# Kernel optimization log

Measured on AMD Instinct MI355X. Metric: run time of the kernel, lower is better.

Reference implementation:

```python
import jax, jax.numpy as jnp
import numpy as np

HEADS = 16  # module init arg `heads`


def setup_inputs() -> dict:
    key = jax.random.key(0)
    k1, k2, k3 = jax.random.split(key, 3)
    B, T, D = 2, 2048, 1024
    x = jax.random.normal(k1, (B, T, D), dtype=jnp.float32)
    w_qkv = jax.random.normal(k2, (D, 3 * D), dtype=jnp.float32) * (1.0 / np.sqrt(D))
    w_proj = jax.random.normal(k3, (D, D), dtype=jnp.float32) * (1.0 / np.sqrt(D))
    b_proj = jnp.zeros((D,), dtype=jnp.float32)
    return {"x": x, "w_qkv": w_qkv, "w_proj": w_proj, "b_proj": b_proj,
            "window": 16, "stride": 16}


def reference(x, w_qkv, w_proj, b_proj, window, stride):
    B, T, D = x.shape
    H = HEADS
    hd = D // H
    scale = 1.0 / np.sqrt(hd)

    qkv = x @ w_qkv                              # [B,T,3D]
    qkv = qkv.reshape(B, T, 3, H, hd)
    q = jnp.transpose(qkv[:, :, 0], (0, 2, 1, 3))  # [B,H,T,hd]
    k = jnp.transpose(qkv[:, :, 1], (0, 2, 1, 3))
    v = jnp.transpose(qkv[:, :, 2], (0, 2, 1, 3))

    # Local window attention: pad front with zeros (matches F.pad), gather
    # sliding windows so patches[..., t, w, :] = k_padded[..., t + w, :].
    pad = window - 1
    k_pad = jnp.pad(k, ((0, 0), (0, 0), (pad, 0), (0, 0)))
    v_pad = jnp.pad(v, ((0, 0), (0, 0), (pad, 0), (0, 0)))
    win_idx = jnp.arange(T)[:, None] + jnp.arange(window)[None, :]  # [T,W]
    pk = k_pad[:, :, win_idx]                    # [B,H,T,W,hd]
    pv = v_pad[:, :, win_idx]                    # [B,H,T,W,hd]

    attn_local = jnp.einsum('bhtd,bhtwd->bhtw', q, pk) * scale
    attn_local = jax.nn.softmax(attn_local, axis=-1)  # zero-pad keys included, as in torch
    out_local = jnp.einsum('bhtw,bhtwd->bhtd', attn_local, pv)

    # Strided global attention
    g_idx = jnp.arange(0, T, stride)
    kg = k[:, :, g_idx]                          # [B,H,G,hd]
    vg = v[:, :, g_idx]
    attn_g = jnp.einsum('bhtd,bhgd->bhtg', q, kg) * scale
    attn_g = jax.nn.softmax(attn_g, axis=-1)
    out_global = jnp.einsum('bhtg,bhgd->bhtd', attn_g, vg)

    out = out_local + out_global                 # [B,H,T,hd]
    out = jnp.transpose(out, (0, 2, 1, 3)).reshape(B, T, D)
    return out @ w_proj + b_proj
```

## Files before the change

kernel.cpp:

```cpp
#include <hip/hip_runtime.h>
#include <hip/hip_bf16.h>

#define BB 2
#define TT 2048
#define DD 1024
#define HH 16
#define HD 64
#define WIN 16
#define NG 128
#define QKVLD 3072

typedef __bf16 bf16x8 __attribute__((ext_vector_type(8)));
typedef _Float16 f16x8 __attribute__((ext_vector_type(8)));
typedef float f32x4 __attribute__((ext_vector_type(4)));
typedef _Float16 h2 __attribute__((ext_vector_type(2)));
typedef __fp16 pk2_t __attribute__((ext_vector_type(2)));

__device__ __forceinline__ unsigned short f2bf(float f) {
    union { float f; unsigned int i; } x; x.f = f;
    unsigned int r = x.i + 0x7FFFu + ((x.i >> 16) & 1u);
    return (unsigned short)(r >> 16);
}
__device__ __forceinline__ unsigned short f2h(float f) {
    union { _Float16 h; unsigned short u; } x; x.h = (_Float16)f; return x.u;
}
__device__ __forceinline__ unsigned int pk2h(float lo, float hi) {
    union { pk2_t h; unsigned int u; } X;
    X.h = __builtin_amdgcn_cvt_pkrtz(lo, hi);
    return X.u;
}

__device__ __forceinline__ void gll16(const unsigned short* g, unsigned short* l) {
    __builtin_amdgcn_global_load_lds(
        (const __attribute__((address_space(1))) void*)g,
        (__attribute__((address_space(3))) void*)l,
        16, 0, 0);
}

__global__ __launch_bounds__(256) void prepass_kernel(
    const float* __restrict__ x,
    const float* __restrict__ w_qkv,
    const float* __restrict__ w_proj,
    unsigned short* __restrict__ xb,
    unsigned short* __restrict__ wqkvT,
    unsigned short* __restrict__ wprojT)
{
    __shared__ float tile[64][65];
    const int bid = blockIdx.x;
    const int tid = threadIdx.x;

    if (bid < 2048) {
        const size_t i = ((size_t)bid * 256 + tid) * 8;
        float4 f0 = *(const float4*)(x + i);
        float4 f1 = *(const float4*)(x + i + 4);
        ushort4 a = { f2bf(f0.x), f2bf(f0.y), f2bf(f0.z), f2bf(f0.w) };
        ushort4 b = { f2bf(f1.x), f2bf(f1.y), f2bf(f1.z), f2bf(f1.w) };
        *(ushort4*)(xb + i) = a;
        *(ushort4*)(xb + i + 4) = b;
        return;
    }

    const float* w;
    unsigned short* wT;
    int nblk, kblk, N;
    if (bid < 2816) {
        const int b2 = bid - 2048;
        w = w_qkv; wT = wqkvT; N = 3072;
        nblk = b2 % 48; kblk = b2 / 48;
    } else {
        const int b2 = bid - 2816;
        w = w_proj; wT = wprojT; N = 1024;
        nblk = b2 % 16; kblk = b2 / 16;
    }
    const int K = 1024;
    const int n0 = nblk * 64, k0 = kblk * 64;

    {
        const int krow = tid >> 2;
        const int nc0  = (tid & 3) * 16;
        const float* src = w + (size_t)(k0 + krow) * N + n0 + nc0;
        float4 f0 = *(const float4*)(src);
        float4 f1 = *(const float4*)(src + 4);
        float4 f2 = *(const float4*)(src + 8);
        float4 f3 = *(const float4*)(src + 12);
        *(float4*)&tile[krow][nc0]      = f0;
        *(float4*)&tile[krow][nc0 + 4]  = f1;
        *(float4*)&tile[krow][nc0 + 8]  = f2;
        *(float4*)&tile[krow][nc0 + 12] = f3;
    }
    __syncthreads();
    #pragma unroll
    for (int rep = 0; rep < 2; ++rep) {
        const int n   = (tid >> 3) + rep * 32;
        const int kc0 = (tid & 7) * 8;
        union { uint4 v; unsigned short u[8]; } o;
        #pragma unroll
        for (int j = 0; j < 8; ++j) o.u[j] = f2bf(tile[kc0 + j][n]);
        *(uint4*)(wT + (size_t)(n0 + n) * K + k0 + kc0) = o.v;
    }
}

template<int MODE, int TN>
__global__ __launch_bounds__(256) void gemm_kernel(
    const unsigned short* __restrict__ A,
    const unsigned short* __restrict__ Bt,
    void* __restrict__ Cp,
    const float* __restrict__ bias,
    int M, int N, int K)
{
    constexpr int NJ = TN / 32;
    constexpr int BRW = TN / 4;
    __shared__ __align__(16) unsigned short As[128 * 64];
    __shared__ __align__(16) unsigned short Bs[TN * 64];
    const int tid  = threadIdx.x;
    const int wave = tid >> 6;
    const int lane = tid & 63;
    const int lm   = lane & 15;
    const int quad = lane >> 4;
    const int wm   = (wave >> 1) * 64;
    const int wn   = (wave & 1) * (TN / 2);
    const int bm   = blockIdx.y * 128;
    const int bn   = blockIdx.x * TN;

    f32x4 acc[4][NJ];
    const f32x4 z4 = { 0.f, 0.f, 0.f, 0.f };
    #pragma unroll
    for (int i = 0; i < 4; ++i)
        #pragma unroll
        for (int j = 0; j < NJ; ++j) acc[i][j] = z4;

    const int lrow = lane >> 3;
    const int lcol = ((lane & 7) ^ lrow) * 8;
    const unsigned short* gA = A  + (size_t)(bm + wave * 32  + lrow) * K + lcol;
    const unsigned short* gB = Bt + (size_t)(bn + wave * BRW + lrow) * K + lcol;
    unsigned short* lA = &As[(wave * 32)  * 64];
    unsigned short* lB = &Bs[(wave * BRW) * 64];

    const int sx = lm & 7;
    for (int k0 = 0; k0 < K; k0 += 64) {
        __syncthreads();
        #pragma unroll
        for (int s = 0; s < 4; ++s)
            gll16(gA + k0 + (size_t)(8 * s) * K, lA + (8 * s) * 64);
        #pragma unroll
        for (int s = 0; s < BRW / 8; ++s)
            gll16(gB + k0 + (size_t)(8 * s) * K, lB + (8 * s) * 64);
        __syncthreads();
        #pragma unroll
        for (int kk = 0; kk < 2; ++kk) {
            bf16x8 af[4], bfr[NJ];
            #pragma unroll
            for (int i = 0; i < 4; ++i)
                af[i] = *(const bf16x8*)&As[(wm + i * 16 + lm) * 64
                                            + (((kk * 4 + quad) ^ sx) * 8)];
            #pragma unroll
            for (int j = 0; j < NJ; ++j)
                bfr[j] = *(const bf16x8*)&Bs[(wn + j * 16 + lm) * 64
                                             + (((kk * 4 + quad) ^ sx) * 8)];
            #pragma unroll
            for (int i = 0; i < 4; ++i)
                #pragma unroll
                for (int j = 0; j < NJ; ++j)
                    acc[i][j] = __builtin_amdgcn_mfma_f32_16x16x32_bf16(
                        af[i], bfr[j], acc[i][j], 0, 0, 0);
        }
    }

    #pragma unroll
    for (int i = 0; i < 4; ++i) {
        #pragma unroll
        for (int r = 0; r < 4; ++r) {
            const int row = bm + wm + i * 16 + quad * 4 + r;
            #pragma unroll
            for (int j = 0; j < NJ; ++j) {
                const int col = bn + wn + j * 16 + lm;
                float v = acc[i][j][r];
                if constexpr (MODE == 0) {
                    ((unsigned short*)Cp)[(size_t)row * N + col] = f2h(v);
                } else {
                    ((float*)Cp)[(size_t)row * N + col] = v + bias[col];
                }
            }
        }
    }
}

__device__ __forceinline__ f16x8 pfrag(unsigned int fa0, unsigned int fa1,
                                       unsigned int fb0, unsigned int fb1,
                                       int quad) {
    const unsigned int t16_0 = (quad == 2) ? fb0 : fa0;
    const unsigned int t16_1 = (quad == 2) ? fb1 : fa1;
    const unsigned int t32_0 = (quad == 0) ? fb0 : fa0;
    const unsigned int t32_1 = (quad == 0) ? fb1 : fa1;
    const unsigned int t48_0 = (quad == 1) ? fb0 : fa0;
    const unsigned int t48_1 = (quad == 1) ? fb1 : fa1;
    const unsigned int s16_0 = (unsigned int)__shfl_xor((int)t16_0, 16, 64);
    const unsigned int s16_1 = (unsigned int)__shfl_xor((int)t16_1, 16, 64);
    const unsigned int s32_0 = (unsigned int)__shfl_xor((int)t32_0, 32, 64);
    const unsigned int s32_1 = (unsigned int)__shfl_xor((int)t32_1, 32, 64);
    const unsigned int s48_0 = (unsigned int)__shfl_xor((int)t48_0, 48, 64);
    const unsigned int s48_1 = (unsigned int)__shfl_xor((int)t48_1, 48, 64);
    unsigned int w0, w1, w2, w3;
    if (quad == 0)      { w0 = fa0;   w1 = fa1;   w2 = s16_0; w3 = s16_1; }
    else if (quad == 1) { w0 = s48_0; w1 = s48_1; w2 = s32_0; w3 = s32_1; }
    else if (quad == 2) { w0 = s32_0; w1 = s32_1; w2 = s48_0; w3 = s48_1; }
    else                { w0 = s16_0; w1 = s16_1; w2 = fb0;   w3 = fb1;   }
    union { unsigned int u[4]; f16x8 v; } R;
    R.u[0] = w0; R.u[1] = w1; R.u[2] = w2; R.u[3] = w3;
    return R.v;
}

__global__ __launch_bounds__(256, 4) void attn_kernel(
    const unsigned short* __restrict__ qkv,
    unsigned short* __restrict__ attn_out)
{
    __shared__ __align__(16) unsigned short smem[14976];
    unsigned short* const Kg  = smem;
    unsigned short* const Kl  = smem + 9216;
    unsigned short* const VgT = smem;
    unsigned short* const VlT = smem + 8704;
    unsigned short* const Ep  = smem + 9216;

    const int tid  = threadIdx.x;
    const int wave = tid >> 6;
    const int lane = tid & 63;
    const int lm   = lane & 15;
    const int quad = lane >> 4;
    const int bx   = blockIdx.x;
    const int bh   = bx >> 5;
    const int t0   = (bx & 31) * 64;
    const int b    = bh >> 4;
    const int h    = bh & 15;

    const size_t baseQ = (size_t)(b * TT) * QKVLD + h * HD;

    const int r  = tid >> 1;
    const int hf = tid & 1;
    uint4 vg[4], vl[4];
    {
        const unsigned short* ks = qkv + baseQ + 1024 + (size_t)(16 * r) * QKVLD + hf * 32;
        const unsigned short* vs = ks + 1024;
        unsigned short* kd = Kg + r * 72 + hf * 32;
        #pragma unroll
        for (int j = 0; j < 4; ++j) *(uint4*)(kd + j * 8) = *(const uint4*)(ks + j * 8);
        #pragma unroll
        for (int j = 0; j < 4; ++j) vg[j] = *(const uint4*)(vs + j * 8);

        if (r < 80) {
            const int tl = t0 - 15 + r;
            unsigned short* kld = Kl + r * 72 + hf * 32;
            if (tl < 0 || tl >= TT) {
                const uint4 z = { 0, 0, 0, 0 };
                #pragma unroll
                for (int j = 0; j < 4; ++j) { *(uint4*)(kld + j * 8) = z; vl[j] = z; }
            } else {
                const unsigned short* kls = qkv + baseQ + 1024 + (size_t)tl * QKVLD + hf * 32;
                const unsigned short* vls = kls + 1024;
                #pragma unroll
                for (int j = 0; j < 4; ++j) *(uint4*)(kld + j * 8) = *(const uint4*)(kls + j * 8);
                #pragma unroll
                for (int j = 0; j < 4; ++j) vl[j] = *(const uint4*)(vls + j * 8);
            }
        }
    }

    f16x8 qf[2];
    {
        const unsigned short* qrow = qkv + baseQ + (size_t)(t0 + 16 * wave + lm) * QKVLD;
        const h2 sc = { (_Float16)0.125f, (_Float16)0.125f };
        #pragma unroll
        for (int c = 0; c < 2; ++c) {
            union { uint4 u; h2 hh[4]; f16x8 v; } U;
            U.u = *(const uint4*)(qrow + c * 32 + quad * 8);
            #pragma unroll
            for (int k = 0; k < 4; ++k) U.hh[k] *= sc;
            qf[c] = U.v;
        }
    }

    __syncthreads();

    f32x4 sg[8], sl[2];
    const f32x4 z4 = { 0.f, 0.f, 0.f, 0.f };
    #pragma unroll
    for (int f = 0; f < 8; ++f) sg[f] = z4;
    sl[0] = z4; sl[1] = z4;
    __builtin_amdgcn_s_setprio(1);
    #pragma unroll
    for (int f = 0; f < 8; ++f)
        #pragma unroll
        for (int c = 0; c < 2; ++c)
            sg[f] = __builtin_amdgcn_mfma_f32_16x16x32_f16(
                *(const f16x8*)&Kg[(16 * f + lm) * 72 + c * 32 + quad * 8], qf[c],
                sg[f], 0, 0, 0);
    #pragma unroll
    for (int f = 0; f < 2; ++f)
        #pragma unroll
        for (int c = 0; c < 2; ++c)
            sl[f] = __builtin_amdgcn_mfma_f32_16x16x32_f16(
                *(const f16x8*)&Kl[(16 * wave + 16 * f + lm) * 72 + c * 32 + quad * 8], qf[c],
                sl[f], 0, 0, 0);
    __builtin_amdgcn_s_setprio(0);

    float invg, invl;
    {
        float dg = 0.f, dl = 0.f;
        #pragma unroll
        for (int f = 0; f < 8; ++f)
            #pragma unroll
            for (int rr = 0; rr < 4; ++rr) {
                float e = __expf(sg[f][rr]); sg[f][rr] = e; dg += e;
            }
        #pragma unroll
        for (int f = 0; f < 2; ++f)
            #pragma unroll
            for (int rr = 0; rr < 4; ++rr) {
                const int j2 = 16 * f + quad * 4 + rr;
                const bool in = (j2 >= lm) && (j2 <= lm + 15);
                float e = in ? __expf(sl[f][rr]) : 0.f;
                sl[f][rr] = e; dl += e;
            }
        dg += __shfl_xor(dg, 16, 64);
        dg += __shfl_xor(dg, 32, 64);
        dl += __shfl_xor(dl, 16, 64);
        dl += __shfl_xor(dl, 32, 64);
        invg = 1.f / dg;
        invl = 1.f / dl;
    }

    f16x8 pa0, pa1, pa2, pa3, pal;
    {
        #pragma unroll
        for (int f = 0; f < 8; ++f)
            #pragma unroll
            for (int rr = 0; rr < 4; ++rr) sg[f][rr] *= invg;
        #pragma unroll
        for (int f = 0; f < 2; ++f)
            #pragma unroll
            for (int rr = 0; rr < 4; ++rr) sl[f][rr] *= invl;
        pa0 = pfrag(pk2h(sg[0][0], sg[0][1]), pk2h(sg[0][2], sg[0][3]),
                    pk2h(sg[1][0], sg[1][1]), pk2h(sg[1][2], sg[1][3]), quad);
        pa1 = pfrag(pk2h(sg[2][0], sg[2][1]), pk2h(sg[2][2], sg[2][3]),
                    pk2h(sg[3][0], sg[3][1]), pk2h(sg[3][2], sg[3][3]), quad);
        pa2 = pfrag(pk2h(sg[4][0], sg[4][1]), pk2h(sg[4][2], sg[4][3]),
                    pk2h(sg[5][0], sg[5][1]), pk2h(sg[5][2], sg[5][3]), quad);
        pa3 = pfrag(pk2h(sg[6][0], sg[6][1]), pk2h(sg[6][2], sg[6][3]),
                    pk2h(sg[7][0], sg[7][1]), pk2h(sg[7][2], sg[7][3]), quad);
        pal = pfrag(pk2h(sl[0][0], sl[0][1]), pk2h(sl[0][2], sl[0][3]),
                    pk2h(sl[1][0], sl[1][1]), pk2h(sl[1][2], sl[1][3]), quad);
    }

    __syncthreads();

    {
        union { uint4 u[4]; unsigned short s[32]; } Ug;
        #pragma unroll
        for (int j = 0; j < 4; ++j) Ug.u[j] = vg[j];
        #pragma unroll
        for (int j = 0; j < 32; ++j) VgT[(hf * 32 + j) * 136 + r] = Ug.s[j];
        if (r < 80) {
            union { uint4 u[4]; unsigned short s[32]; } Ul;
            #pragma unroll
            for (int j = 0; j < 4; ++j) Ul.u[j] = vl[j];
            #pragma unroll
            for (int j = 0; j < 32; ++j) VlT[(hf * 32 + j) * 88 + r] = Ul.s[j];
        }
    }

    __syncthreads();

    f32x4 o[4];
    #pragma unroll
    for (int c = 0; c < 4; ++c) o[c] = z4;
    __builtin_amdgcn_s_setprio(1);
    #pragma unroll
    for (int c = 0; c < 4; ++c) {
        o[c] = __builtin_amdgcn_mfma_f32_16x16x32_f16(
            pa0, *(const f16x8*)&VgT[(16 * c + lm) * 136 + 0 * 32 + quad * 8], o[c], 0, 0, 0);
        o[c] = __builtin_amdgcn_mfma_f32_16x16x32_f16(
            pa1, *(const f16x8*)&VgT[(16 * c + lm) * 136 + 1 * 32 + quad * 8], o[c], 0, 0, 0);
        o[c] = __builtin_amdgcn_mfma_f32_16x16x32_f16(
            pa2, *(const f16x8*)&VgT[(16 * c + lm) * 136 + 2 * 32 + quad * 8], o[c], 0, 0, 0);
        o[c] = __builtin_amdgcn_mfma_f32_16x16x32_f16(
            pa3, *(const f16x8*)&VgT[(16 * c + lm) * 136 + 3 * 32 + quad * 8], o[c], 0, 0, 0);
        o[c] = __builtin_amdgcn_mfma_f32_16x16x32_f16(
            pal, *(const f16x8*)&VlT[(16 * c + lm) * 88 + 16 * wave + quad * 8], o[c], 0, 0, 0);
    }
    __builtin_amdgcn_s_setprio(0);

    __syncthreads();

    {
        unsigned short* const Pw = Ep + wave * (16 * 72);
        #pragma unroll
        for (int rr = 0; rr < 4; ++rr) {
            unsigned short* orow_p = Pw + (quad * 4 + rr) * 72;
            #pragma unroll
            for (int c = 0; c < 4; ++c) orow_p[16 * c + lm] = f2bf(o[c][rr]);
        }
        const int orow = lane >> 2;
        const int ocol = (lane & 3) * 16;
        const uint4 d0 = *(const uint4*)&Pw[orow * 72 + ocol];
        const uint4 d1 = *(const uint4*)&Pw[orow * 72 + ocol + 8];
        unsigned short* dst = attn_out + (size_t)(b * TT + t0 + 16 * wave + orow) * DD + h * HD + ocol;
        *(uint4*)(dst)     = d0;
        *(uint4*)(dst + 8) = d1;
    }
}

extern "C" void kernel_launch(void* const* d_in, const int* in_sizes, int n_in,
                              void* d_out, int out_size, void* d_ws, size_t ws_size,
                              hipStream_t stream) {
    const float* x      = (const float*)d_in[0];
    const float* w_qkv  = (const float*)d_in[1];
    const float* w_proj = (const float*)d_in[2];
    const float* b_proj = (const float*)d_in[3];

    char* ws = (char*)d_ws;
    unsigned short* qkv    = (unsigned short*)ws;
    unsigned short* xb     = (unsigned short*)(ws + 25165824);
    unsigned short* attnb  = xb;
    unsigned short* wqkvT  = (unsigned short*)(ws + 25165824 + 8388608);
    unsigned short* wprojT = (unsigned short*)(ws + 25165824 + 8388608 + 6291456);
    float* out = (float*)d_out;

    prepass_kernel<<<3072, 256, 0, stream>>>(x, w_qkv, w_proj, xb, wqkvT, wprojT);

    gemm_kernel<0, 128><<<dim3(3072 / 128, 4096 / 128), 256, 0, stream>>>(
        xb, wqkvT, qkv, nullptr, 4096, 3072, 1024);

    attn_kernel<<<dim3(BB * HH * (TT / 64)), 256, 0, stream>>>(qkv, attnb);

    gemm_kernel<1, 64><<<dim3(1024 / 64, 4096 / 128), 256, 0, stream>>>(
        attnb, wprojT, out, b_proj, 4096, 1024, 1024);
}
```

Baseline: 148.7 us.

## Double attention query block to 128 rows with 512 threads; widen proj GEMM tile

The attention kernel now processes 128 query rows per block with 8 waves instead of 64 rows with 4 waves. The global strided K/V tile is then loaded and transposed once for twice as many queries, which halves redundant global-key traffic. Local K/V staging is split across thread halves, and an extra 16-row tail is loaded by the first 32 threads. The output projection GEMM also moves from a 64 to a 128 N-tile, leaving fewer blocks (256 instead of 512), which may reduce occupancy and load balance.

```diff
diff --git a/kernel.cpp b/kernel.cpp
--- a/kernel.cpp
+++ b/kernel.cpp
@@ -9,6 +9,7 @@
 #define WIN 16
 #define NG 128
 #define QKVLD 3072
+#define QB 128
 
 typedef __bf16 bf16x8 __attribute__((ext_vector_type(8)));
 typedef _Float16 f16x8 __attribute__((ext_vector_type(8)));
@@ -210,16 +211,16 @@
     return R.v;
 }
 
-__global__ __launch_bounds__(256, 4) void attn_kernel(
+__global__ __launch_bounds__(512, 4) void attn_kernel(
     const unsigned short* __restrict__ qkv,
     unsigned short* __restrict__ attn_out)
 {
-    __shared__ __align__(16) unsigned short smem[14976];
+    __shared__ __align__(16) unsigned short smem[19584];
     unsigned short* const Kg  = smem;
     unsigned short* const Kl  = smem + 9216;
     unsigned short* const VgT = smem;
-    unsigned short* const VlT = smem + 8704;
-    unsigned short* const Ep  = smem + 9216;
+    unsigned short* const VlT = smem + 9216;
+    unsigned short* const Ep  = smem;
 
     const int tid  = threadIdx.x;
     const int wave = tid >> 6;
@@ -227,40 +228,52 @@
     const int lm   = lane & 15;
     const int quad = lane >> 4;
     const int bx   = blockIdx.x;
-    const int bh   = bx >> 5;
-    const int t0   = (bx & 31) * 64;
+    const int bh   = bx >> 4;
+    const int t0   = (bx & 15) * QB;
     const int b    = bh >> 4;
     const int h    = bh & 15;
 
     const size_t baseQ = (size_t)(b * TT) * QKVLD + h * HD;
 
-    const int r  = tid >> 1;
+    const int r  = (tid & 255) >> 1;
     const int hf = tid & 1;
-    uint4 vg[4], vl[4];
-    {
+    uint4 va[4];
+    if (tid < 256) {
         const unsigned short* ks = qkv + baseQ + 1024 + (size_t)(16 * r) * QKVLD + hf * 32;
         const unsigned short* vs = ks + 1024;
         unsigned short* kd = Kg + r * 72 + hf * 32;
         #pragma unroll
         for (int j = 0; j < 4; ++j) *(uint4*)(kd + j * 8) = *(const uint4*)(ks + j * 8);
         #pragma unroll
-        for (int j = 0; j < 4; ++j) vg[j] = *(const uint4*)(vs + j * 8);
-
-        if (r < 80) {
-            const int tl = t0 - 15 + r;
-            unsigned short* kld = Kl + r * 72 + hf * 32;
-            if (tl < 0 || tl >= TT) {
-                const uint4 z = { 0, 0, 0, 0 };
-                #pragma unroll
-                for (int j = 0; j < 4; ++j) { *(uint4*)(kld + j * 8) = z; vl[j] = z; }
-            } else {
-                const unsigned short* kls = qkv + baseQ + 1024 + (size_t)tl * QKVLD + hf * 32;
-                const unsigned short* vls = kls + 1024;
-                #pragma unroll
-                for (int j = 0; j < 4; ++j) *(uint4*)(kld + j * 8) = *(const uint4*)(kls + j * 8);
-                #pragma unroll
-                for (int j = 0; j < 4; ++j) vl[j] = *(const uint4*)(vls + j * 8);
-            }
+        for (int j = 0; j < 4; ++j) va[j] = *(const uint4*)(vs + j * 8);
+    } else {
+        const int tl = t0 - 15 + r;
+        unsigned short* kld = Kl + r * 72 + hf * 32;
+        if (tl < 0 || tl >= TT) {
+            const uint4 z = { 0, 0, 0, 0 };
+            #pragma unroll
+            for (int j = 0; j < 4; ++j) { *(uint4*)(kld + j * 8) = z; va[j] = z; }
+        } else {
+            const unsigned short* kls = qkv + baseQ + 1024 + (size_t)tl * QKVLD + hf * 32;
+            const unsigned short* vls = kls + 1024;
+            #pragma unroll
+            for (int j = 0; j < 4; ++j) *(uint4*)(kld + j * 8) = *(const uint4*)(kls + j * 8);
+            #pragma unroll
+            for (int j = 0; j < 4; ++j) va[j] = *(const uint4*)(vls + j * 8);
+        }
+    }
+    if (tid < 32) {
+        const int r2 = 128 + (tid >> 1);
+        const int tl = t0 - 15 + r2;
+        unsigned short* kld = Kl + r2 * 72 + hf * 32;
+        if (tl < 0 || tl >= TT) {
+            const uint4 z = { 0, 0, 0, 0 };
+            #pragma unroll
+            for (int j = 0; j < 4; ++j) *(uint4*)(kld + j * 8) = z;
+        } else {
+            const unsigned short* kls = qkv + baseQ + 1024 + (size_t)tl * QKVLD + hf * 32;
+            #pragma unroll
+            for (int j = 0; j < 4; ++j) *(uint4*)(kld + j * 8) = *(const uint4*)(kls + j * 8);
         }
     }
 
@@ -353,17 +366,31 @@
     __syncthreads();
 
     {
-        union { uint4 u[4]; unsigned short s[32]; } Ug;
-        #pragma unroll
-        for (int j = 0; j < 4; ++j) Ug.u[j] = vg[j];
-        #pragma unroll
-        for (int j = 0; j < 32; ++j) VgT[(hf * 32 + j) * 136 + r] = Ug.s[j];
-        if (r < 80) {
-            union { uint4 u[4]; unsigned short s[32]; } Ul;
-            #pragma unroll
-            for (int j = 0; j < 4; ++j) Ul.u[j] = vl[j];
-            #pragma unroll
-            for (int j = 0; j < 32; ++j) VlT[(hf * 32 + j) * 88 + r] = Ul.s[j];
+        union { uint4 u[4]; unsigned short s[32]; } U;
+        #pragma unroll
+        for (int j = 0; j < 4; ++j) U.u[j] = va[j];
+        if (tid < 256) {
+            #pragma unroll
+            for (int j = 0; j < 32; ++j) VgT[(hf * 32 + j) * 136 + r] = U.s[j];
+        } else {
+            #pragma unroll
+            for (int j = 0; j < 32; ++j) VlT[(hf * 32 + j) * 152 + r] = U.s[j];
+        }
+        if (tid < 32) {
+            const int r2 = 128 + (tid >> 1);
+            const int tl = t0 - 15 + r2;
+            union { uint4 u[4]; unsigned short s[32]; } W;
+            if (tl < 0 || tl >= TT) {
+                const uint4 z = { 0, 0, 0, 0 };
+                #pragma unroll
+                for (int j = 0; j < 4; ++j) W.u[j] = z;
+            } else {
+                const unsigned short* vls = qkv + baseQ + 2048 + (size_t)tl * QKVLD + hf * 32;
+                #pragma unroll
+                for (int j = 0; j < 4; ++j) W.u[j] = *(const uint4*)(vls + j * 8);
+            }
+            #pragma unroll
+            for (int j = 0; j < 32; ++j) VlT[(hf * 32 + j) * 152 + r2] = W.s[j];
         }
     }
 
@@ -384,7 +411,7 @@
         o[c] = __builtin_amdgcn_mfma_f32_16x16x32_f16(
             pa3, *(const f16x8*)&VgT[(16 * c + lm) * 136 + 3 * 32 + quad * 8], o[c], 0, 0, 0);
         o[c] = __builtin_amdgcn_mfma_f32_16x16x32_f16(
-            pal, *(const f16x8*)&VlT[(16 * c + lm) * 88 + 16 * wave + quad * 8], o[c], 0, 0, 0);
+            pal, *(const f16x8*)&VlT[(16 * c + lm) * 152 + 16 * wave + quad * 8], o[c], 0, 0, 0);
     }
     __builtin_amdgcn_s_setprio(0);
 
@@ -429,8 +456,8 @@
     gemm_kernel<0, 128><<<dim3(3072 / 128, 4096 / 128), 256, 0, stream>>>(
         xb, wqkvT, qkv, nullptr, 4096, 3072, 1024);
 
-    attn_kernel<<<dim3(BB * HH * (TT / 64)), 256, 0, stream>>>(qkv, attnb);
-
-    gemm_kernel<1, 64><<<dim3(1024 / 64, 4096 / 128), 256, 0, stream>>>(
+    attn_kernel<<<dim3(BB * HH * (TT / QB)), 512, 0, stream>>>(qkv, attnb);
+
+    gemm_kernel<1, 128><<<dim3(1024 / 128, 4096 / 128), 256, 0, stream>>>(
         attnb, wprojT, out, b_proj, 4096, 1024, 1024);
 }
```

Measured after the change: 157.2 us. 5.7% more time.
